# Kernel optimization log

Hardware: AMD Instinct MI355X
Metric: run time of the kernel (lower is better)

The kernel has to match this reference:

```python
import jax, jax.numpy as jnp
import numpy as np

DX = 1.0      # grid spacing
RHO = 1.0     # density
NU = 0.1      # viscosity
DT = 0.1      # timestep
STEPS = 1000  # Jacobi relaxation iterations

# Periodic (CIRCULAR) finite-difference stencils via jnp.roll on the last two axes.

def ddx(f):
    # central difference along x (axis -2)
    return (jnp.roll(f, -1, axis=-2) - jnp.roll(f, 1, axis=-2)) / (2.0 * DX)

def ddy(f):
    # central difference along y (axis -1)
    return (jnp.roll(f, -1, axis=-1) - jnp.roll(f, 1, axis=-1)) / (2.0 * DX)

def neighbor_sum(f):
    # 4-neighbor sum: LapInv stencil used by the Jacobi step
    return (jnp.roll(f, 1, axis=-2) + jnp.roll(f, -1, axis=-2)
            + jnp.roll(f, 1, axis=-1) + jnp.roll(f, -1, axis=-1))

def laplacian(f):
    # 5-point Laplacian / dx^2
    return (neighbor_sum(f) - 4.0 * f) / (DX * DX)


def setup_inputs() -> dict:
    key = jax.random.key(0)
    k1, k2 = jax.random.split(key)
    X = jax.random.normal(k1, (2, 1, 512, 512), dtype=jnp.float32)
    forcing = jax.random.normal(k2, (2, 1, 512, 512), dtype=jnp.float32)
    t = jnp.zeros((), dtype=jnp.float32)
    return {"t": t, "X": X, "forcing": forcing}


def reference(t, X, forcing):
    # advection (v . grad) v : X[0]*dXi/dx + X[1]*dXi/dy, broadcast over vector dim
    adv = X[0] * ddx(X) + X[1] * ddy(X)              # (2, C, H, W)
    partial = -adv + NU * laplacian(X) + forcing      # (2, C, H, W)
    # divergence of partial -> pressure Poisson RHS
    B = RHO * (ddx(partial[0]) + ddy(partial[1])) / DT  # (C, H, W)

    def poisson_jacobi_step(phi, _):
        phi = (neighbor_sum(phi) - B * (DX * DX)) / 4.0
        return phi, None

    phi, _ = jax.lax.scan(poisson_jacobi_step, B, xs=None, length=STEPS)
    grad_phi = jnp.stack([ddx(phi), ddy(phi)])        # (2, C, H, W)
    return partial - grad_phi / RHO
```

## Files before the change

kernel.cpp:

```cpp
#include <hip/hip_runtime.h>
#include <math.h>


#define HH 512
#define WW 512
#define NCELL (HH * WW)
#define NU_C 0.1f
#define PI_F 3.14159265358979323846f
#define PADDED 576

__device__ __forceinline__ int padi(int i) { return i + (i >> 3); }

__device__ __forceinline__ float2 cadd(float2 a, float2 b) { return make_float2(a.x + b.x, a.y + b.y); }
__device__ __forceinline__ float2 csub(float2 a, float2 b) { return make_float2(a.x - b.x, a.y - b.y); }
__device__ __forceinline__ float2 cmul(float2 a, float2 b) {
    return make_float2(a.x * b.x - a.y * b.y, a.x * b.y + a.y * b.x);
}

template <int S>
__device__ __forceinline__ float2 cmul_tw(float2 a, float2 w) {
    float wy = (S < 0) ? w.y : -w.y;
    return make_float2(a.x * w.x - a.y * wy, a.x * wy + a.y * w.x);
}

template <int S>
__device__ __forceinline__ void bfly8(float2 r[8]) {
    const float c = 0.70710678118654752f;
    const float s = (float)S;
    float2 e0 = cadd(r[0], r[4]), f0 = csub(r[0], r[4]);
    float2 e1 = cadd(r[2], r[6]), f1 = csub(r[2], r[6]);
    float2 g0 = cadd(r[1], r[5]), h0 = csub(r[1], r[5]);
    float2 g1 = cadd(r[3], r[7]), h1 = csub(r[3], r[7]);
    float2 E0 = cadd(e0, e1), E2 = csub(e0, e1);
    float2 if1 = make_float2(-s * f1.y, s * f1.x);
    float2 E1 = cadd(f0, if1), E3 = csub(f0, if1);
    float2 O0 = cadd(g0, g1), O2 = csub(g0, g1);
    float2 ih1 = make_float2(-s * h1.y, s * h1.x);
    float2 O1 = cadd(h0, ih1), O3 = csub(h0, ih1);
    float2 t1 = make_float2(c * (O1.x - s * O1.y), c * (O1.y + s * O1.x));
    float2 t2 = make_float2(-s * O2.y, s * O2.x);
    float2 t3 = make_float2(-c * (O3.x + s * O3.y), -c * (O3.y - s * O3.x));
    r[0] = cadd(E0, O0); r[4] = csub(E0, O0);
    r[1] = cadd(E1, t1); r[5] = csub(E1, t1);
    r[2] = cadd(E2, t2); r[6] = csub(E2, t2);
    r[3] = cadd(E3, t3); r[7] = csub(E3, t3);
}

struct Twid { float2 s1[8]; float2 s2[8]; };

__device__ __forceinline__ void make_tw(Twid& tw, int t) {
    float sn, cs;
    sincosf(-2.0f * PI_F * (float)(t & 7) * (1.0f / 64.0f), &sn, &cs);
    float2 T1 = make_float2(cs, sn);
    tw.s1[0] = make_float2(1.0f, 0.0f);
#pragma unroll
    for (int m = 1; m < 8; ++m) tw.s1[m] = cmul(tw.s1[m - 1], T1);
    sincosf(-2.0f * PI_F * (float)t * (1.0f / 512.0f), &sn, &cs);
    float2 T2 = make_float2(cs, sn);
    tw.s2[0] = make_float2(1.0f, 0.0f);
#pragma unroll
    for (int m = 1; m < 8; ++m) tw.s2[m] = cmul(tw.s2[m - 1], T2);
}

template <int S>
__device__ __forceinline__ void fft512(float2 r[8], const Twid& tw,
                                       float2* b0, float2* b1, int t) {
    bfly8<S>(r);
#pragma unroll
    for (int k = 0; k < 8; ++k) b0[padi(8 * t + k)] = r[k];
    __syncthreads();
#pragma unroll
    for (int m = 0; m < 8; ++m) r[m] = b0[padi(t + 64 * m)];
#pragma unroll
    for (int m = 1; m < 8; ++m) r[m] = cmul_tw<S>(r[m], tw.s1[m]);
    bfly8<S>(r);
    int base = ((t >> 3) << 6) + (t & 7);
#pragma unroll
    for (int k = 0; k < 8; ++k) b1[padi(base + 8 * k)] = r[k];
    __syncthreads();
#pragma unroll
    for (int m = 0; m < 8; ++m) r[m] = b1[padi(t + 64 * m)];
#pragma unroll
    for (int m = 1; m < 8; ++m) r[m] = cmul_tw<S>(r[m], tw.s2[m]);
    bfly8<S>(r);
}

__global__ __launch_bounds__(64) void kA(const float* __restrict__ X,
                                         const float* __restrict__ F,
                                         float* __restrict__ p,
                                         float2* __restrict__ Zt) {
    __shared__ float2 b0[PADDED], b1[PADDED];
    int i = blockIdx.x, t = threadIdx.x;
    Twid tw; make_tw(tw, t);
    int ip = (i + 1) & 511, im = (i + 511) & 511;
    const float* X0 = X;
    const float* X1 = X + NCELL;
    float2 r[8];
#pragma unroll
    for (int m = 0; m < 8; ++m) {
        int j = t + 64 * m;
        int jp = (j + 1) & 511, jm = (j + 511) & 511;
        float x0c = X0[i * WW + j], x1c = X1[i * WW + j];
        float aip = X0[ip * WW + j], aim = X0[im * WW + j];
        float ajp = X0[i * WW + jp], ajm = X0[i * WW + jm];
        float p0 = -(x0c * (aip - aim) * 0.5f + x1c * (ajp - ajm) * 0.5f)
                 + NU_C * (aip + aim + ajp + ajm - 4.0f * x0c) + F[i * WW + j];
        float bip = X1[ip * WW + j], bim = X1[im * WW + j];
        float bjp = X1[i * WW + jp], bjm = X1[i * WW + jm];
        float p1 = -(x0c * (bip - bim) * 0.5f + x1c * (bjp - bjm) * 0.5f)
                 + NU_C * (bip + bim + bjp + bjm - 4.0f * x1c) + F[NCELL + i * WW + j];
        p[i * WW + j] = p0;
        p[NCELL + i * WW + j] = p1;
        r[m] = make_float2(p0, p1);
    }
    fft512<-1>(r, tw, b0, b1, t);
#pragma unroll
    for (int k = 0; k < 8; ++k) Zt[(t + 64 * k) * 512 + i] = r[k];
}

__global__ __launch_bounds__(64) void kB(const float2* __restrict__ Zt,
                                         float2* __restrict__ W1) {
    __shared__ float2 b0[PADDED], b1[PADDED], zbuf[512];
    int j = blockIdx.x, t = threadIdx.x;
    int mj = (WW - j) & 511;
    Twid tw; make_tw(tw, t);
    float2 r[8];

#pragma unroll
    for (int m = 0; m < 8; ++m) r[m] = Zt[mj * 512 + t + 64 * m];
    fft512<-1>(r, tw, b0, b1, t);
#pragma unroll
    for (int k = 0; k < 8; ++k) zbuf[t + 64 * k] = r[k];
    __syncthreads();

#pragma unroll
    for (int m = 0; m < 8; ++m) r[m] = Zt[j * 512 + t + 64 * m];
    fft512<-1>(r, tw, b0, b1, t);

    float shy, chy;
    sincosf(PI_F * (float)j * (1.0f / 512.0f), &shy, &chy);
    float sy = 2.0f * shy * chy;
    float qy = shy * shy;
#pragma unroll
    for (int k = 0; k < 8; ++k) {
        int ki = t + 64 * k;
        int mi = (HH - ki) & 511;
        float shx, chx;
        sincosf(PI_F * (float)ki * (1.0f / 512.0f), &shx, &chx);
        float sx = 2.0f * shx * chx;
        float qx = shx * shx;
        float qs = qx + qy;
        float beta = 0.0f;
        if (ki != 0 || j != 0) {
            float rN;
            if (qs < 1.0f)      rN = expf(1000.0f * log1pf(-qs));
            else if (qs > 1.0f) rN = expf(1000.0f * logf(qs - 1.0f));
            else                rN = 0.0f;
            float M = rN - (1.0f - rN) / (4.0f * qs);
            beta = -10.0f * M * (1.0f / (512.0f * 512.0f));
        }
        float su  = sx * sx + sy * sy;
        float u2x = sx * sx - sy * sy;
        float u2y = 2.0f * sx * sy;
        float2 z  = r[k];
        float2 zc = zbuf[mi];
        float cx = zc.x, cy = -zc.y;
        float tx = u2x * cx - u2y * cy;
        float ty = u2x * cy + u2y * cx;
        float bh = 0.5f * beta;
        r[k] = make_float2(bh * (su * z.x + tx), bh * (su * z.y + ty));
    }
    __syncthreads();

    fft512<1>(r, tw, b0, b1, t);
#pragma unroll
    for (int k = 0; k < 8; ++k) W1[(t + 64 * k) * 512 + j] = r[k];
}

__global__ __launch_bounds__(64) void kC(const float2* __restrict__ W1,
                                         const float* __restrict__ p,
                                         float* __restrict__ out) {
    __shared__ float2 b0[PADDED], b1[PADDED];
    int i = blockIdx.x, t = threadIdx.x;
    Twid tw; make_tw(tw, t);
    float2 r[8];
#pragma unroll
    for (int m = 0; m < 8; ++m) r[m] = W1[i * 512 + t + 64 * m];
    fft512<1>(r, tw, b0, b1, t);
#pragma unroll
    for (int k = 0; k < 8; ++k) {
        int j = t + 64 * k;
        float2 w = r[k];
        out[i * WW + j]         = p[i * WW + j]         - w.x;
        out[NCELL + i * WW + j] = p[NCELL + i * WW + j] - w.y;
    }
}

extern "C" void kernel_launch(void* const* d_in, const int* in_sizes, int n_in,
                              void* d_out, int out_size, void* d_ws, size_t ws_size,
                              hipStream_t stream) {
    const float* X = (const float*)d_in[1];
    const float* F = (const float*)d_in[2];
    float* out = (float*)d_out;
    float* ws  = (float*)d_ws;

    float*  p  = ws;
    float2* Zt = (float2*)(ws + 2 * NCELL);
    float2* W1 = Zt + NCELL;

    kA<<<dim3(512), dim3(64), 0, stream>>>(X, F, p, Zt);
    kB<<<dim3(512), dim3(64), 0, stream>>>(Zt, W1);
    kC<<<dim3(512), dim3(64), 0, stream>>>(W1, p, out);
}
```

Before: 82.97 us.

## Split spectral solve kernel and pair rows for coalesced transposed writes

Kernel kB, which ran the column FFT twice (once for the mirrored column), is split into kB1, which does each column FFT once and stores the spectrum, and kB2, which applies the spectral multiplier using the mirrored entries and runs the inverse FFT. kA and kB2 now process two rows per 128-thread block and stage the results through shared memory, so the transposed stores go out as float4 pairs. kB2 also advances the per-element sincos with a rotation recurrence instead of calling sincosf each time. This removes the duplicate FFT work and the strided 8-byte scatter writes. In exchange it adds a kernel launch and a full extra spectrum round-trip through global memory, and the rotation recurrence can accumulate rounding drift.

```diff
diff --git a/kernel.cpp b/kernel.cpp
--- a/kernel.cpp
+++ b/kernel.cpp
@@ -85,12 +85,14 @@
     bfly8<S>(r);
 }
 
-__global__ __launch_bounds__(64) void kA(const float* __restrict__ X,
-                                         const float* __restrict__ F,
-                                         float* __restrict__ p,
-                                         float2* __restrict__ Zt) {
-    __shared__ float2 b0[PADDED], b1[PADDED];
-    int i = blockIdx.x, t = threadIdx.x;
+__global__ __launch_bounds__(128) void kA(const float* __restrict__ X,
+                                          const float* __restrict__ F,
+                                          float* __restrict__ p,
+                                          float2* __restrict__ Zt) {
+    __shared__ float2 b0[2][PADDED], b1[2][PADDED];
+    int b = blockIdx.x;
+    int w = threadIdx.x >> 6, t = threadIdx.x & 63;
+    int i = 2 * b + w;
     Twid tw; make_tw(tw, t);
     int ip = (i + 1) & 511, im = (i + 511) & 511;
     const float* X0 = X;
@@ -113,42 +115,59 @@
         p[NCELL + i * WW + j] = p1;
         r[m] = make_float2(p0, p1);
     }
-    fft512<-1>(r, tw, b0, b1, t);
-#pragma unroll
-    for (int k = 0; k < 8; ++k) Zt[(t + 64 * k) * 512 + i] = r[k];
-}
-
-__global__ __launch_bounds__(64) void kB(const float2* __restrict__ Zt,
-                                         float2* __restrict__ W1) {
-    __shared__ float2 b0[PADDED], b1[PADDED], zbuf[512];
+    fft512<-1>(r, tw, b0[w], b1[w], t);
+#pragma unroll
+    for (int k = 0; k < 8; ++k) b0[w][t + 64 * k] = r[k];
+    __syncthreads();
+#pragma unroll
+    for (int q = 0; q < 4; ++q) {
+        int f = threadIdx.x + 128 * q;
+        float2 v0 = b0[0][f], v1 = b0[1][f];
+        *reinterpret_cast<float4*>(&Zt[f * 512 + 2 * b]) = make_float4(v0.x, v0.y, v1.x, v1.y);
+    }
+}
+
+__global__ __launch_bounds__(64) void kB1(const float2* __restrict__ Zt,
+                                          float2* __restrict__ S) {
+    __shared__ float2 b0[PADDED], b1[PADDED];
     int j = blockIdx.x, t = threadIdx.x;
-    int mj = (WW - j) & 511;
-    Twid tw; make_tw(tw, t);
-    float2 r[8];
-
-#pragma unroll
-    for (int m = 0; m < 8; ++m) r[m] = Zt[mj * 512 + t + 64 * m];
-    fft512<-1>(r, tw, b0, b1, t);
-#pragma unroll
-    for (int k = 0; k < 8; ++k) zbuf[t + 64 * k] = r[k];
-    __syncthreads();
-
+    Twid tw; make_tw(tw, t);
+    float2 r[8];
 #pragma unroll
     for (int m = 0; m < 8; ++m) r[m] = Zt[j * 512 + t + 64 * m];
     fft512<-1>(r, tw, b0, b1, t);
+#pragma unroll
+    for (int k = 0; k < 8; ++k) S[j * 512 + t + 64 * k] = r[k];
+}
+
+__global__ __launch_bounds__(128) void kB2(const float2* __restrict__ S,
+                                           float2* __restrict__ W1) {
+    __shared__ float2 b0[2][PADDED], b1[2][PADDED];
+    int b = blockIdx.x;
+    int w = threadIdx.x >> 6, t = threadIdx.x & 63;
+    int j = 2 * b + w;
+    int mj = (512 - j) & 511;
+    Twid tw; make_tw(tw, t);
 
     float shy, chy;
     sincosf(PI_F * (float)j * (1.0f / 512.0f), &shy, &chy);
     float sy = 2.0f * shy * chy;
     float qy = shy * shy;
+
+    float sh, ch;
+    sincosf(PI_F * (float)t * (1.0f / 512.0f), &sh, &ch);
+    const float c8 = 0.92387953251128675613f;
+    const float s8 = 0.38268343236508977173f;
+
+    float2 r[8];
 #pragma unroll
     for (int k = 0; k < 8; ++k) {
         int ki = t + 64 * k;
         int mi = (HH - ki) & 511;
-        float shx, chx;
-        sincosf(PI_F * (float)ki * (1.0f / 512.0f), &shx, &chx);
-        float sx = 2.0f * shx * chx;
-        float qx = shx * shx;
+        float2 z  = S[j * 512 + ki];
+        float2 zc = S[mj * 512 + mi];
+        float sx = 2.0f * sh * ch;
+        float qx = sh * sh;
         float qs = qx + qy;
         float beta = 0.0f;
         if (ki != 0 || j != 0) {
@@ -162,19 +181,26 @@
         float su  = sx * sx + sy * sy;
         float u2x = sx * sx - sy * sy;
         float u2y = 2.0f * sx * sy;
-        float2 z  = r[k];
-        float2 zc = zbuf[mi];
         float cx = zc.x, cy = -zc.y;
         float tx = u2x * cx - u2y * cy;
         float ty = u2x * cy + u2y * cx;
         float bh = 0.5f * beta;
         r[k] = make_float2(bh * (su * z.x + tx), bh * (su * z.y + ty));
-    }
-    __syncthreads();
-
-    fft512<1>(r, tw, b0, b1, t);
-#pragma unroll
-    for (int k = 0; k < 8; ++k) W1[(t + 64 * k) * 512 + j] = r[k];
+        float nch = ch * c8 - sh * s8;
+        sh = sh * c8 + ch * s8;
+        ch = nch;
+    }
+
+    fft512<1>(r, tw, b0[w], b1[w], t);
+#pragma unroll
+    for (int k = 0; k < 8; ++k) b0[w][t + 64 * k] = r[k];
+    __syncthreads();
+#pragma unroll
+    for (int q = 0; q < 4; ++q) {
+        int f = threadIdx.x + 128 * q;
+        float2 v0 = b0[0][f], v1 = b0[1][f];
+        *reinterpret_cast<float4*>(&W1[f * 512 + 2 * b]) = make_float4(v0.x, v0.y, v1.x, v1.y);
+    }
 }
 
 __global__ __launch_bounds__(64) void kC(const float2* __restrict__ W1,
@@ -206,9 +232,11 @@
 
     float*  p  = ws;
     float2* Zt = (float2*)(ws + 2 * NCELL);
-    float2* W1 = Zt + NCELL;
-
-    kA<<<dim3(512), dim3(64), 0, stream>>>(X, F, p, Zt);
-    kB<<<dim3(512), dim3(64), 0, stream>>>(Zt, W1);
-    kC<<<dim3(512), dim3(64), 0, stream>>>(W1, p, out);
-}
+    float2* S  = Zt + NCELL;
+    float2* W1 = S + NCELL;
+
+    kA <<<dim3(256), dim3(128), 0, stream>>>(X, F, p, Zt);
+    kB1<<<dim3(512), dim3(64),  0, stream>>>(Zt, S);
+    kB2<<<dim3(256), dim3(128), 0, stream>>>(S, W1);
+    kC <<<dim3(512), dim3(64),  0, stream>>>(W1, p, out);
+}
```

After: 77.94 us. -6.1%, faster.

## Pair conjugate columns in one block and move transposes to strided reads

Applied to the files above, without the earlier changes.

kB now runs 256 blocks of two wavefronts, each handling column j and its conjugate partner 512-j. Each column is FFT'd once and the two share the result through LDS, replacing the old scheme that computed the mirror column's FFT redundantly. Row and column transposes are moved from strided writes to strided reads in kB and kC. Per-k sincos in the spectral multiply is replaced by a rotation recurrence, and kC prefetches p before its FFT. Strided reads may coalesce poorly, and the recurrence adds a little float rounding error.

```diff
diff --git a/kernel.cpp b/kernel.cpp
--- a/kernel.cpp
+++ b/kernel.cpp
@@ -115,43 +115,44 @@
     }
     fft512<-1>(r, tw, b0, b1, t);
 #pragma unroll
-    for (int k = 0; k < 8; ++k) Zt[(t + 64 * k) * 512 + i] = r[k];
-}
-
-__global__ __launch_bounds__(64) void kB(const float2* __restrict__ Zt,
-                                         float2* __restrict__ W1) {
-    __shared__ float2 b0[PADDED], b1[PADDED], zbuf[512];
-    int j = blockIdx.x, t = threadIdx.x;
-    int mj = (WW - j) & 511;
+    for (int k = 0; k < 8; ++k) Zt[i * 512 + t + 64 * k] = r[k];
+}
+
+__global__ __launch_bounds__(128) void kB(const float2* __restrict__ Zt,
+                                          float2* __restrict__ W1) {
+    __shared__ float2 b0[2][PADDED], b1[2][PADDED];
+    const int b = blockIdx.x;
+    const int w = threadIdx.x >> 6, t = threadIdx.x & 63;
+    const int cw = (b == 0) ? (w ? 256 : 0) : (w ? 512 - b : b);
+    const int mw = (b == 0) ? w : (w ^ 1);
     Twid tw; make_tw(tw, t);
     float2 r[8];
-
-#pragma unroll
-    for (int m = 0; m < 8; ++m) r[m] = Zt[mj * 512 + t + 64 * m];
-    fft512<-1>(r, tw, b0, b1, t);
-#pragma unroll
-    for (int k = 0; k < 8; ++k) zbuf[t + 64 * k] = r[k];
-    __syncthreads();
-
-#pragma unroll
-    for (int m = 0; m < 8; ++m) r[m] = Zt[j * 512 + t + 64 * m];
-    fft512<-1>(r, tw, b0, b1, t);
+#pragma unroll
+    for (int m = 0; m < 8; ++m) r[m] = Zt[(t + 64 * m) * 512 + cw];
+    fft512<-1>(r, tw, b0[w], b1[w], t);
+#pragma unroll
+    for (int k = 0; k < 8; ++k) b0[w][t + 64 * k] = r[k];
+    __syncthreads();
 
     float shy, chy;
-    sincosf(PI_F * (float)j * (1.0f / 512.0f), &shy, &chy);
+    sincosf(PI_F * (float)cw * (1.0f / 512.0f), &shy, &chy);
     float sy = 2.0f * shy * chy;
     float qy = shy * shy;
+    float sh, ch;
+    sincosf(PI_F * (float)t * (1.0f / 512.0f), &sh, &ch);
+    const float c8 = 0.92387953251128675613f;
+    const float s8 = 0.38268343236508977173f;
 #pragma unroll
     for (int k = 0; k < 8; ++k) {
         int ki = t + 64 * k;
         int mi = (HH - ki) & 511;
-        float shx, chx;
-        sincosf(PI_F * (float)ki * (1.0f / 512.0f), &shx, &chx);
-        float sx = 2.0f * shx * chx;
-        float qx = shx * shx;
+        float2 z  = r[k];
+        float2 zc = b0[mw][mi];
+        float sx = 2.0f * sh * ch;
+        float qx = sh * sh;
         float qs = qx + qy;
         float beta = 0.0f;
-        if (ki != 0 || j != 0) {
+        if (ki != 0 || cw != 0) {
             float rN;
             if (qs < 1.0f)      rN = expf(1000.0f * log1pf(-qs));
             else if (qs > 1.0f) rN = expf(1000.0f * logf(qs - 1.0f));
@@ -162,19 +163,19 @@
         float su  = sx * sx + sy * sy;
         float u2x = sx * sx - sy * sy;
         float u2y = 2.0f * sx * sy;
-        float2 z  = r[k];
-        float2 zc = zbuf[mi];
         float cx = zc.x, cy = -zc.y;
         float tx = u2x * cx - u2y * cy;
         float ty = u2x * cy + u2y * cx;
         float bh = 0.5f * beta;
         r[k] = make_float2(bh * (su * z.x + tx), bh * (su * z.y + ty));
-    }
-    __syncthreads();
-
-    fft512<1>(r, tw, b0, b1, t);
-#pragma unroll
-    for (int k = 0; k < 8; ++k) W1[(t + 64 * k) * 512 + j] = r[k];
+        float nch = ch * c8 - sh * s8;
+        sh = sh * c8 + ch * s8;
+        ch = nch;
+    }
+    __syncthreads();
+    fft512<1>(r, tw, b0[w], b1[w], t);
+#pragma unroll
+    for (int k = 0; k < 8; ++k) W1[cw * 512 + t + 64 * k] = r[k];
 }
 
 __global__ __launch_bounds__(64) void kC(const float2* __restrict__ W1,
@@ -183,16 +184,21 @@
     __shared__ float2 b0[PADDED], b1[PADDED];
     int i = blockIdx.x, t = threadIdx.x;
     Twid tw; make_tw(tw, t);
+    float pp0[8], pp1[8];
+#pragma unroll
+    for (int k = 0; k < 8; ++k) {
+        pp0[k] = p[i * WW + t + 64 * k];
+        pp1[k] = p[NCELL + i * WW + t + 64 * k];
+    }
     float2 r[8];
 #pragma unroll
-    for (int m = 0; m < 8; ++m) r[m] = W1[i * 512 + t + 64 * m];
+    for (int m = 0; m < 8; ++m) r[m] = W1[(t + 64 * m) * 512 + i];
     fft512<1>(r, tw, b0, b1, t);
 #pragma unroll
     for (int k = 0; k < 8; ++k) {
         int j = t + 64 * k;
-        float2 w = r[k];
-        out[i * WW + j]         = p[i * WW + j]         - w.x;
-        out[NCELL + i * WW + j] = p[NCELL + i * WW + j] - w.y;
+        out[i * WW + j]         = pp0[k] - r[k].x;
+        out[NCELL + i * WW + j] = pp1[k] - r[k].y;
     }
 }
 
@@ -208,7 +214,7 @@
     float2* Zt = (float2*)(ws + 2 * NCELL);
     float2* W1 = Zt + NCELL;
 
-    kA<<<dim3(512), dim3(64), 0, stream>>>(X, F, p, Zt);
-    kB<<<dim3(512), dim3(64), 0, stream>>>(Zt, W1);
-    kC<<<dim3(512), dim3(64), 0, stream>>>(W1, p, out);
-}
+    kA<<<dim3(512), dim3(64),  0, stream>>>(X, F, p, Zt);
+    kB<<<dim3(256), dim3(128), 0, stream>>>(Zt, W1);
+    kC<<<dim3(512), dim3(64),  0, stream>>>(W1, p, out);
+}
```

Measured after the change: 78.79 us. 5.0% less time.
